# Kernel tuning notes

Hardware: AMD Instinct MI355X
Metric: run time of the kernel (lower is better)

The kernel has to match this reference:

```python
import jax, jax.numpy as jnp
import numpy as np

N, DIM, TOPK = 8192, 512, 10


def setup_inputs() -> dict:
    key = jax.random.key(0)
    k1, k2, k3, k4, k5 = jax.random.split(key, 5)
    s = DIM ** -0.5
    return {
        "X": jax.random.normal(k1, (N, DIM), dtype=jnp.float32),
        "Wh": jax.random.normal(k2, (DIM, DIM), dtype=jnp.float32) * s,
        "bh": jax.random.normal(k3, (DIM,), dtype=jnp.float32) * s,
        "Wt": jax.random.normal(k4, (DIM, DIM), dtype=jnp.float32) * s,
        "bt": jax.random.normal(k5, (DIM,), dtype=jnp.float32) * s,
    }


def reference(X, Wh, bh, Wt, bt):
    n, dim = X.shape
    scale = dim ** -0.5
    e_h = X @ Wh.T + bh                      # [n, dim]
    e_t = X @ Wt.T + bt                      # [n, dim]
    logits = (e_h @ e_t.T) * scale           # [n, n]
    topk_val, topk_idx = jax.lax.top_k(logits, TOPK)   # [n, k]
    weights = jax.nn.softmax(topk_val, axis=-1)        # [n, k]
    src = jnp.repeat(jnp.arange(n, dtype=jnp.int32), TOPK)  # [n*k]
    dst = topk_idx.reshape(-1).astype(jnp.int32)
    edge_index = jnp.stack([src, dst], axis=0)          # [2, n*k]
    edge_weight = weights.reshape(-1)                   # [n*k]
    return edge_index, edge_weight
```

## Files before the change

### kernel.cpp

```cpp
#include <hip/hip_runtime.h>
#include <math.h>

#define NROWS 8192
#define DIMK  512
#define TOPK  10
#define SCALE 0.044194173824159223f

#define ETM 128
#define ETN 128
#define ETK 32
#define NTHREADS 256

#define BM 128
#define BN 128
#define BK 32
#define NS2 16
#define SCOLS2 (NROWS / NS2)
#define NQ 256
#define CAP 64
#define TMARGIN 2.0f

typedef __attribute__((ext_vector_type(8))) short bf16x8;
typedef __attribute__((ext_vector_type(4))) float f32x4;
typedef __attribute__((ext_vector_type(2))) float f32x2;

__device__ __forceinline__ unsigned short f2bf(float f) {
  unsigned int u = __float_as_uint(f);
  u = (u + 0x7FFF + ((u >> 16) & 1)) >> 16;
  return (unsigned short)u;
}

__device__ __forceinline__ void gld16(const void* g, const void* lds) {
  __builtin_amdgcn_global_load_lds(
      (const __attribute__((address_space(1))) void*)g,
      (__attribute__((address_space(3))) void*)lds, 16, 0, 0);
}

__device__ __forceinline__ f32x2 pk_fma(f32x2 a, f32x2 b, f32x2 c) {
#if __has_builtin(__builtin_elementwise_fma)
  return __builtin_elementwise_fma(a, b, c);
#else
  f32x2 r; r[0] = fmaf(a[0], b[0], c[0]); r[1] = fmaf(a[1], b[1], c[1]);
  return r;
#endif
}

__global__ __launch_bounds__(NTHREADS, 2)
void embed_gemm(const float* __restrict__ X,
                const float* __restrict__ Wh, const float* __restrict__ bh,
                const float* __restrict__ Wt, const float* __restrict__ bt,
                float* __restrict__ Eh, float* __restrict__ Et,
                unsigned short* __restrict__ Ehb, unsigned short* __restrict__ Etb) {
  __shared__ float As[2][ETK][ETM + 4];
  __shared__ float Bs[2][ETK][ETN + 4];

  const int tid = threadIdx.x;
  const int rowBase = blockIdx.x * ETM;
  const int colBase = blockIdx.y * ETN;
  const float* W  = (colBase < DIMK) ? Wh : Wt;
  const float* bb = (colBase < DIMK) ? bh : bt;
  float* Out            = (colBase < DIMK) ? Eh : Et;
  unsigned short* Outb  = (colBase < DIMK) ? Ehb : Etb;
  const int colOff = colBase & (DIMK - 1);

  const int tx = tid & 15, ty = tid >> 4;
  f32x2 acc2[8][4];
#pragma unroll
  for (int r = 0; r < 8; ++r)
#pragma unroll
    for (int p = 0; p < 4; ++p) acc2[r][p] = (f32x2){0.f, 0.f};

  auto stage = [&](int buf, int kt) {
#pragma unroll
    for (int u = 0; u < 4; ++u) {
      const int idx = tid + u * NTHREADS;
      const int r = idx >> 3;
      const int dc = idx & 7;
      const float4 av = *(const float4*)&X[(size_t)(rowBase + r) * DIMK + kt + dc * 4];
      As[buf][dc * 4 + 0][r] = av.x; As[buf][dc * 4 + 1][r] = av.y;
      As[buf][dc * 4 + 2][r] = av.z; As[buf][dc * 4 + 3][r] = av.w;
    }
#pragma unroll
    for (int u = 0; u < 4; ++u) {
      const int idx = tid + u * NTHREADS;
      const int r = idx >> 3;
      const int dc = idx & 7;
      const float4 bv = *(const float4*)&W[(size_t)(colOff + r) * DIMK + kt + dc * 4];
      Bs[buf][dc * 4 + 0][r] = bv.x; Bs[buf][dc * 4 + 1][r] = bv.y;
      Bs[buf][dc * 4 + 2][r] = bv.z; Bs[buf][dc * 4 + 3][r] = bv.w;
    }
  };
  auto compute = [&](int buf) {
#pragma unroll 4
    for (int k = 0; k < ETK; ++k) {
      const float4 a0 = *(const float4*)&As[buf][k][ty * 4];
      const float4 a1 = *(const float4*)&As[buf][k][64 + ty * 4];
      const float4 b0 = *(const float4*)&Bs[buf][k][tx * 4];
      const float4 b1 = *(const float4*)&Bs[buf][k][64 + tx * 4];
      const float ar[8] = {a0.x, a0.y, a0.z, a0.w, a1.x, a1.y, a1.z, a1.w};
      const f32x2 bp[4] = {(f32x2){b0.x, b0.y}, (f32x2){b0.z, b0.w},
                           (f32x2){b1.x, b1.y}, (f32x2){b1.z, b1.w}};
#pragma unroll
      for (int r = 0; r < 8; ++r) {
        const f32x2 ar2 = (f32x2){ar[r], ar[r]};
#pragma unroll
        for (int p = 0; p < 4; ++p)
          acc2[r][p] = pk_fma(ar2, bp[p], acc2[r][p]);
      }
    }
  };

  stage(0, 0);
  __syncthreads();
#pragma unroll 1
  for (int ki = 0; ki < DIMK / ETK; ki += 2) {
    if (ki + 1 < DIMK / ETK) stage(1, (ki + 1) * ETK);
    compute(0);
    __syncthreads();
    if (ki + 2 < DIMK / ETK) stage(0, (ki + 2) * ETK);
    compute(1);
    __syncthreads();
  }

  float br[8];
  {
    const float4 bv0 = *(const float4*)&bb[colOff + tx * 4];
    const float4 bv1 = *(const float4*)&bb[colOff + 64 + tx * 4];
    br[0] = bv0.x; br[1] = bv0.y; br[2] = bv0.z; br[3] = bv0.w;
    br[4] = bv1.x; br[5] = bv1.y; br[6] = bv1.z; br[7] = bv1.w;
  }
#pragma unroll
  for (int r = 0; r < 8; ++r) {
    const int row = rowBase + ((r < 4) ? (ty * 4 + r) : (64 + ty * 4 + r - 4));
    float4 o0, o1;
    o0.x = acc2[r][0][0] + br[0]; o0.y = acc2[r][0][1] + br[1];
    o0.z = acc2[r][1][0] + br[2]; o0.w = acc2[r][1][1] + br[3];
    o1.x = acc2[r][2][0] + br[4]; o1.y = acc2[r][2][1] + br[5];
    o1.z = acc2[r][3][0] + br[6]; o1.w = acc2[r][3][1] + br[7];
    const size_t off0 = (size_t)row * DIMK + colOff + tx * 4;
    const size_t off1 = off0 + 64;
    *(float4*)&Out[off0] = o0;
    *(float4*)&Out[off1] = o1;
    ushort4 q0, q1;
    q0.x = f2bf(o0.x); q0.y = f2bf(o0.y); q0.z = f2bf(o0.z); q0.w = f2bf(o0.w);
    q1.x = f2bf(o1.x); q1.y = f2bf(o1.y); q1.z = f2bf(o1.z); q1.w = f2bf(o1.w);
    *(ushort4*)&Outb[off0] = q0;
    *(ushort4*)&Outb[off1] = q1;
  }
}

__global__ __launch_bounds__(256, 3)
void screen_store(const unsigned short* __restrict__ Ehb,
                  const unsigned short* __restrict__ Etb,
                  float* __restrict__ tmax, unsigned short* __restrict__ Sc) {
  __shared__ unsigned short As[2][BM * BK];
  __shared__ unsigned short Bs[2][BN * BK];
  __shared__ unsigned short Csb[BM * 72];

  const int tid = threadIdx.x;
  const int rowBase = blockIdx.x * BM;
  const int strip = blockIdx.y;
  const int w = tid >> 6, lane = tid & 63;
  const int q = lane >> 4, l15 = lane & 15;
  const int wr = (w & 1) * 64, wc = (w >> 1) * 64;
  const int rr = tid >> 1, hq = tid & 1;

  const int c0 = tid, c1 = tid + 256;
  const int wb0 = __builtin_amdgcn_readfirstlane(tid & ~63);
  const int wb1 = wb0 + 256;
  const int ar0 = c0 >> 2, ac0 = (c0 & 3) * 8;
  const int ar1 = c1 >> 2, ac1 = (c1 & 3) * 8;

  for (int ct = 0; ct < SCOLS2; ct += BN) {
    const int colBase = strip * SCOLS2 + ct;
    const int tileG = colBase >> 7;
    f32x4 acc[4][4];
#pragma unroll
    for (int i = 0; i < 4; ++i)
#pragma unroll
      for (int j = 0; j < 4; ++j) acc[i][j] = (f32x4){0.f, 0.f, 0.f, 0.f};

    auto stage = [&](int buf, int kt) {
      gld16(Ehb + (size_t)(rowBase + ar0) * DIMK + kt + ac0, As[buf] + wb0 * 8);
      gld16(Ehb + (size_t)(rowBase + ar1) * DIMK + kt + ac1, As[buf] + wb1 * 8);
      gld16(Etb + (size_t)(colBase + ar0) * DIMK + kt + ac0, Bs[buf] + wb0 * 8);
      gld16(Etb + (size_t)(colBase + ar1) * DIMK + kt + ac1, Bs[buf] + wb1 * 8);
    };
    auto compute = [&](int buf) {
      bf16x8 af[4], bf[4];
#pragma unroll
      for (int i = 0; i < 4; ++i)
        af[i] = *(const bf16x8*)&As[buf][(wr + i * 16 + l15) * BK + q * 8];
#pragma unroll
      for (int j = 0; j < 4; ++j)
        bf[j] = *(const bf16x8*)&Bs[buf][(wc + j * 16 + l15) * BK + q * 8];
#pragma unroll
      for (int i = 0; i < 4; ++i)
#pragma unroll
        for (int j = 0; j < 4; ++j)
          acc[i][j] = __builtin_amdgcn_mfma_f32_16x16x32_bf16(af[i], bf[j], acc[i][j], 0, 0, 0);
    };

    stage(0, 0);
    __syncthreads();
#pragma unroll 1
    for (int ki = 0; ki < DIMK / BK; ki += 2) {
      if (ki + 1 < DIMK / BK) stage(1, (ki + 1) * BK);
      compute(0);
      __syncthreads();
      if (ki + 2 < DIMK / BK) stage(0, (ki + 2) * BK);
      compute(1);
      __syncthreads();
    }

#pragma unroll
    for (int half = 0; half < 2; ++half) {
      if ((w >> 1) == half) {
#pragma unroll
        for (int i = 0; i < 4; ++i)
#pragma unroll
          for (int j = 0; j < 4; ++j)
#pragma unroll
            for (int rg = 0; rg < 4; ++rg)
              Csb[(wr + i * 16 + q * 4 + rg) * 72 + j * 16 + l15] = f2bf(acc[i][j][rg]);
      }
      __syncthreads();
      float m = -INFINITY;
      uint4 buf4[4];
#pragma unroll
      for (int k = 0; k < 4; ++k) {
        buf4[k] = *(const uint4*)&Csb[rr * 72 + hq * 32 + k * 8];
        const unsigned int uu[4] = {buf4[k].x, buf4[k].y, buf4[k].z, buf4[k].w};
#pragma unroll
        for (int e = 0; e < 4; ++e) {
          m = fmaxf(m, __uint_as_float(uu[e] << 16));
          m = fmaxf(m, __uint_as_float(uu[e] & 0xFFFF0000u));
        }
      }
      tmax[(size_t)(rowBase + rr) * NQ + tileG * 4 + half * 2 + hq] = m;
      uint4* dst = (uint4*)&Sc[(size_t)(rowBase + rr) * NROWS + colBase + half * 64 + hq * 32];
#pragma unroll
      for (int k = 0; k < 4; ++k) dst[k] = buf4[k];
      __syncthreads();
    }
  }
}

__global__ __launch_bounds__(256)
void collect_rescore(const unsigned short* __restrict__ Sc,
                     const float* __restrict__ tmax,
                     const float* __restrict__ Eh, const float* __restrict__ Et,
                     float* __restrict__ out) {
  __shared__ int lcnt;
  __shared__ int lcand[CAP];
  const int lane = threadIdx.x & 63;
  const int wid = threadIdx.x >> 6;
  const int r = blockIdx.x;

  if (threadIdx.x == 0) lcnt = 0;
  __syncthreads();

  const f32x4 gm = *(const f32x4*)&tmax[(size_t)r * NQ + lane * 4];
  float a0 = gm[0], a1 = gm[1], a2 = gm[2], a3 = gm[3];
  float g = -INFINITY;
#pragma unroll 1
  for (int j = 0; j < TOPK; ++j) {
    const float lm = fmaxf(fmaxf(a0, a1), fmaxf(a2, a3));
    g = lm;
#pragma unroll
    for (int off = 32; off > 0; off >>= 1) g = fmaxf(g, __shfl_xor(g, off, 64));
    const unsigned long long ball = __ballot(lm == g);
    const int src = __ffsll((long long)ball) - 1;
    if (lane == src) {
      if      (a0 == g) a0 = -INFINITY;
      else if (a1 == g) a1 = -INFINITY;
      else if (a2 == g) a2 = -INFINITY;
      else              a3 = -INFINITY;
    }
  }
  const float tt = g - TMARGIN;

  const unsigned short* row = Sc + (size_t)r * NROWS;
#pragma unroll 1
  for (int it = 0; it < 4; ++it) {
    const int cc0 = (wid * 4 + it) * 512 + lane * 8;
    const uint4 u = *(const uint4*)&row[cc0];
    const unsigned int uu[4] = {u.x, u.y, u.z, u.w};
#pragma unroll
    for (int e = 0; e < 4; ++e) {
      const float lo = __uint_as_float(uu[e] << 16);
      const float hi = __uint_as_float(uu[e] & 0xFFFF0000u);
      if (lo >= tt) {
        const int p = atomicAdd(&lcnt, 1);
        if (p < CAP) lcand[p] = cc0 + 2 * e;
      }
      if (hi >= tt) {
        const int p = atomicAdd(&lcnt, 1);
        if (p < CAP) lcand[p] = cc0 + 2 * e + 1;
      }
    }
  }
  __syncthreads();
  if (wid != 0) return;

  const int n = min(lcnt, CAP);
  const bool active = lane < n;
  const int col = active ? lcand[lane] : 0;

  const float* a = Eh + (size_t)r * DIMK;
  const float* b = Et + (size_t)col * DIMK;
  float p = 0.f;
#pragma unroll 4
  for (int k = 0; k < DIMK; k += 4) {
    const float4 av = *(const float4*)&a[k];
    const float4 bv = *(const float4*)&b[k];
    p = fmaf(av.x, bv.x, p);
    p = fmaf(av.y, bv.y, p);
    p = fmaf(av.z, bv.z, p);
    p = fmaf(av.w, bv.w, p);
  }
  float v = active ? p * SCALE : -INFINITY;
  const int vc = active ? col : 0x7FFFFFFF;

  float myv = -INFINITY; int myc = 0; float m = 0.f;
  float vv = v; int cc2 = vc;
#pragma unroll 1
  for (int j = 0; j < TOPK; ++j) {
    float bvv = vv; int bcc = cc2;
#pragma unroll
    for (int off = 32; off > 0; off >>= 1) {
      const float ov = __shfl_xor(bvv, off, 64);
      const int oc = __shfl_xor(bcc, off, 64);
      if (ov > bvv || (ov == bvv && oc < bcc)) { bvv = ov; bcc = oc; }
    }
    if (j == 0) m = bvv;
    if (lane == j) { myv = bvv; myc = bcc; }
    if (vv == bvv && cc2 == bcc) vv = -INFINITY;
  }

  float sum = 0.f;
#pragma unroll
  for (int j = 0; j < TOPK; ++j) sum += expf(__shfl(myv, j, 64) - m);
  const float inv = 1.0f / sum;

  if (lane < TOPK) {
    const size_t ro = (size_t)r * TOPK + lane;
    out[ro] = (float)r;
    out[(size_t)NROWS * TOPK + ro] = (float)myc;
    out[2 * (size_t)NROWS * TOPK + ro] = expf(myv - m) * inv;
  }
}

extern "C" void kernel_launch(void* const* d_in, const int* in_sizes, int n_in,
                              void* d_out, int out_size, void* d_ws, size_t ws_size,
                              hipStream_t stream) {
  const float* X  = (const float*)d_in[0];
  const float* Wh = (const float*)d_in[1];
  const float* bh = (const float*)d_in[2];
  const float* Wt = (const float*)d_in[3];
  const float* bt = (const float*)d_in[4];
  float* out = (float*)d_out;

  char* ws = (char*)d_ws;
  const size_t embB  = (size_t)NROWS * DIMK * sizeof(float);
  const size_t embBH = (size_t)NROWS * DIMK * sizeof(unsigned short);
  const size_t tmaxB = (size_t)NROWS * NQ * sizeof(float);
  float* Eh   = (float*)ws;
  float* Et   = (float*)(ws + embB);
  unsigned short* Ehb = (unsigned short*)(ws + 2 * embB);
  unsigned short* Etb = (unsigned short*)(ws + 2 * embB + embBH);
  float* tmax = (float*)(ws + 2 * embB + 2 * embBH);
  unsigned short* Sc = (unsigned short*)(ws + 2 * embB + 2 * embBH + tmaxB);

  dim3 blk(NTHREADS);
  dim3 g1(NROWS / ETM, (2 * DIMK) / ETN);
  embed_gemm<<<g1, blk, 0, stream>>>(X, Wh, bh, Wt, bt, Eh, Et, Ehb, Etb);

  dim3 g2(NROWS / BM, NS2);
  screen_store<<<g2, blk, 0, stream>>>(Ehb, Etb, tmax, Sc);

  collect_rescore<<<NROWS, blk, 0, stream>>>(Sc, tmax, Eh, Et, out);
}
```

Measured before the change: 381.6 us.

## Widen screening GEMM tile to 128x256 with 8 MFMA columns per wave

```diff
diff --git a/kernel.cpp b/kernel.cpp
--- a/kernel.cpp
+++ b/kernel.cpp
@@ -12,9 +12,9 @@
 #define NTHREADS 256
 
 #define BM 128
-#define BN 128
+#define BN 256
 #define BK 32
-#define NS2 16
+#define NS2 8
 #define SCOLS2 (NROWS / NS2)
 #define NQ 256
 #define CAP 64
@@ -149,7 +149,7 @@
   }
 }
 
-__global__ __launch_bounds__(256, 3)
+__global__ __launch_bounds__(256, 2)
 void screen_store(const unsigned short* __restrict__ Ehb,
                   const unsigned short* __restrict__ Etb,
                   float* __restrict__ tmax, unsigned short* __restrict__ Sc) {
@@ -162,42 +162,43 @@
   const int strip = blockIdx.y;
   const int w = tid >> 6, lane = tid & 63;
   const int q = lane >> 4, l15 = lane & 15;
-  const int wr = (w & 1) * 64, wc = (w >> 1) * 64;
+  const int wr = (w & 1) * 64, wc = (w >> 1) * 128;
   const int rr = tid >> 1, hq = tid & 1;
 
-  const int c0 = tid, c1 = tid + 256;
   const int wb0 = __builtin_amdgcn_readfirstlane(tid & ~63);
-  const int wb1 = wb0 + 256;
-  const int ar0 = c0 >> 2, ac0 = (c0 & 3) * 8;
-  const int ar1 = c1 >> 2, ac1 = (c1 & 3) * 8;
+  const int ar0 = tid >> 2,        ac0 = (tid & 3) * 8;
+  const int ar1 = (tid + 256) >> 2, ac1 = ((tid + 256) & 3) * 8;
 
   for (int ct = 0; ct < SCOLS2; ct += BN) {
     const int colBase = strip * SCOLS2 + ct;
-    const int tileG = colBase >> 7;
-    f32x4 acc[4][4];
+    f32x4 acc[4][8];
 #pragma unroll
     for (int i = 0; i < 4; ++i)
 #pragma unroll
-      for (int j = 0; j < 4; ++j) acc[i][j] = (f32x4){0.f, 0.f, 0.f, 0.f};
+      for (int j = 0; j < 8; ++j) acc[i][j] = (f32x4){0.f, 0.f, 0.f, 0.f};
 
     auto stage = [&](int buf, int kt) {
       gld16(Ehb + (size_t)(rowBase + ar0) * DIMK + kt + ac0, As[buf] + wb0 * 8);
-      gld16(Ehb + (size_t)(rowBase + ar1) * DIMK + kt + ac1, As[buf] + wb1 * 8);
-      gld16(Etb + (size_t)(colBase + ar0) * DIMK + kt + ac0, Bs[buf] + wb0 * 8);
-      gld16(Etb + (size_t)(colBase + ar1) * DIMK + kt + ac1, Bs[buf] + wb1 * 8);
+      gld16(Ehb + (size_t)(rowBase + ar1) * DIMK + kt + ac1, As[buf] + (wb0 + 256) * 8);
+#pragma unroll
+      for (int u = 0; u < 4; ++u) {
+        const int c = tid + u * 256;
+        gld16(Etb + (size_t)(colBase + (c >> 2)) * DIMK + kt + (c & 3) * 8,
+              Bs[buf] + (wb0 + u * 256) * 8);
+      }
     };
     auto compute = [&](int buf) {
-      bf16x8 af[4], bf[4];
+      bf16x8 af[4], bf[8];
 #pragma unroll
       for (int i = 0; i < 4; ++i)
         af[i] = *(const bf16x8*)&As[buf][(wr + i * 16 + l15) * BK + q * 8];
 #pragma unroll
-      for (int j = 0; j < 4; ++j)
+      for (int j = 0; j < 8; ++j)
         bf[j] = *(const bf16x8*)&Bs[buf][(wc + j * 16 + l15) * BK + q * 8];
 #pragma unroll
       for (int i = 0; i < 4; ++i)
 #pragma unroll
-        for (int j = 0; j < 4; ++j)
+        for (int j = 0; j < 8; ++j)
           acc[i][j] = __builtin_amdgcn_mfma_f32_16x16x32_bf16(af[i], bf[j], acc[i][j], 0, 0, 0);
     };
 
@@ -214,15 +215,17 @@
     }
 
 #pragma unroll
-    for (int half = 0; half < 2; ++half) {
-      if ((w >> 1) == half) {
+    for (int qtr = 0; qtr < 4; ++qtr) {
+      const int jbase = (qtr & 1) * 4;
+      if ((w >> 1) == (qtr >> 1)) {
 #pragma unroll
         for (int i = 0; i < 4; ++i)
 #pragma unroll
-          for (int j = 0; j < 4; ++j)
+          for (int jj = 0; jj < 4; ++jj)
 #pragma unroll
             for (int rg = 0; rg < 4; ++rg)
-              Csb[(wr + i * 16 + q * 4 + rg) * 72 + j * 16 + l15] = f2bf(acc[i][j][rg]);
+              Csb[(wr + i * 16 + q * 4 + rg) * 72 + jj * 16 + l15] =
+                  f2bf(acc[i][jbase + jj][rg]);
       }
       __syncthreads();
       float m = -INFINITY;
@@ -237,8 +240,9 @@
           m = fmaxf(m, __uint_as_float(uu[e] & 0xFFFF0000u));
         }
       }
-      tmax[(size_t)(rowBase + rr) * NQ + tileG * 4 + half * 2 + hq] = m;
-      uint4* dst = (uint4*)&Sc[(size_t)(rowBase + rr) * NROWS + colBase + half * 64 + hq * 32];
+      const int gbase = (colBase + qtr * 64) >> 5;
+      tmax[(size_t)(rowBase + rr) * NQ + gbase + hq] = m;
+      uint4* dst = (uint4*)&Sc[(size_t)(rowBase + rr) * NROWS + colBase + qtr * 64 + hq * 32];
 #pragma unroll
       for (int k = 0; k < 4; ++k) dst[k] = buf4[k];
       __syncthreads();
```

New measurement: 368.7 us. -3.4%, faster.
